# Optimization experiments

Hardware: AMD Instinct MI355X
Metric: run time of the kernel (lower is better)

## Reference

```python
import jax, jax.numpy as jnp
import numpy as np

N, E, G = 100000, 800000, 1000
N_IN, NHID, HEADS, NOUT = 128, 32, 4, 768
HC = NHID * HEADS


def setup_inputs() -> dict:
    key = jax.random.key(0)
    ks = jax.random.split(key, 12)
    s = 1.0 / np.sqrt(N_IN)
    inp = {
        "x": jax.random.normal(ks[0], (N, N_IN), jnp.float32),
        "edge_index": jax.random.randint(ks[1], (2, E), 0, N, jnp.int64),
        "batch": jnp.sort(jax.random.randint(ks[2], (N,), 0, G, jnp.int64)),
        "Wq": jax.random.uniform(ks[3], (N_IN, HC), jnp.float32, -s, s),
        "bq": jnp.zeros((HC,), jnp.float32),
        "Wk": jax.random.uniform(ks[4], (N_IN, HC), jnp.float32, -s, s),
        "bk": jnp.zeros((HC,), jnp.float32),
        "Wv": jax.random.uniform(ks[5], (N_IN, HC), jnp.float32, -s, s),
        "bv": jnp.zeros((HC,), jnp.float32),
        "Wskip": jax.random.uniform(ks[6], (N_IN, HC), jnp.float32, -s, s),
        "bskip": jnp.zeros((HC,), jnp.float32),
        "Wbeta": jax.random.uniform(ks[7], (3 * HC, 1), jnp.float32, -1.0 / np.sqrt(3 * HC), 1.0 / np.sqrt(3 * HC)),
        "W2": jax.random.uniform(ks[8], (HC, NOUT), jnp.float32, -1.0 / np.sqrt(HC), 1.0 / np.sqrt(HC)),
        "b2": jnp.zeros((NOUT,), jnp.float32),
    }
    return inp


def _transformer_net(x, edge_index, batch, Wq, bq, Wk, bk, Wv, bv, Wskip, bskip, Wbeta, W2, b2):
    src, dst = edge_index[0], edge_index[1]  # messages src -> dst
    q = (x @ Wq + bq).reshape(N, HEADS, NHID)
    k = (x @ Wk + bk).reshape(N, HEADS, NHID)
    v = (x @ Wv + bv).reshape(N, HEADS, NHID)
    # edge-wise attention logits [E, H]
    alpha = jnp.einsum('ehc,ehc->eh', q[dst], k[src]) / np.sqrt(NHID)
    # segment softmax over incoming edges of each destination node
    m = jax.ops.segment_max(alpha, dst, num_segments=N)  # [N, H]
    e = jnp.exp(alpha - m[dst])
    denom = jax.ops.segment_sum(e, dst, num_segments=N)  # [N, H]
    attn = e / (denom[dst] + 1e-16)  # [E, H]
    msg = v[src] * attn[..., None]  # [E, H, C]
    out = jax.ops.segment_sum(msg, dst, num_segments=N).reshape(N, HC)
    # beta gating (root skip)
    skip = x @ Wskip + bskip  # [N, HC]
    beta = jax.nn.sigmoid(jnp.concatenate([out, skip, out - skip], axis=-1) @ Wbeta)  # [N, 1]
    out = beta * skip + (1.0 - beta) * out
    # LeakyReLU (default slope 0.01)
    out = jnp.where(out >= 0, out, 0.01 * out)
    # global mean pool per graph
    sums = jax.ops.segment_sum(out, batch, num_segments=G)  # [G, HC]
    cnts = jax.ops.segment_sum(jnp.ones((N,), out.dtype), batch, num_segments=G)
    pooled = sums / jnp.maximum(cnts, 1.0)[:, None]
    return pooled @ W2 + b2  # [G, NOUT]


def reference(x, edge_index, batch, Wq, bq, Wk, bk, Wv, bv, Wskip, bskip, Wbeta, W2, b2):
    return _transformer_net(x, edge_index, batch, Wq, bq, Wk, bk, Wv, bv, Wskip, bskip, Wbeta, W2, b2)
```

## Files before the change

### kernel.cpp

```cpp
#include <hip/hip_runtime.h>
#include <hip/hip_bf16.h>
#include <math.h>

#define NIN 128
#define HC 128
#define NOUT 768

typedef __attribute__((ext_vector_type(8))) short bf16x8;
typedef __attribute__((ext_vector_type(4))) float f32x4;
typedef __attribute__((ext_vector_type(4))) unsigned short ushort4v;
typedef __attribute__((ext_vector_type(8))) unsigned short ushort8v;

__device__ __forceinline__ unsigned short f2bf(float f) {
    __hip_bfloat16 h = __float2bfloat16(f);
    return *(unsigned short*)&h;
}

__device__ __forceinline__ float bfe(ushort8v u, int j) {
    return __uint_as_float(((unsigned int)u[j]) << 16);
}

__global__ __launch_bounds__(256) void prep_w(
    const float* __restrict__ Wq, const float* __restrict__ Wk,
    const float* __restrict__ Wv, const float* __restrict__ Wsk,
    unsigned short* __restrict__ Wtb)
{
    const float* W = (blockIdx.x == 0) ? Wq : (blockIdx.x == 1) ? Wk
                   : (blockIdx.x == 2) ? Wv : Wsk;
    unsigned short* out = Wtb + (size_t)blockIdx.x * 128 * 128;
    const int t = threadIdx.x;
    for (int s = 0; s < 16; ++s) {
        const int f = t + s * 256;
        const int k = f >> 5;
        const int n = (f & 31) * 4;
        float4 w4 = *(const float4*)(W + (size_t)k * 128 + n);
        out[(size_t)(n    ) * 128 + k] = f2bf(w4.x);
        out[(size_t)(n + 1) * 128 + k] = f2bf(w4.y);
        out[(size_t)(n + 2) * 128 + k] = f2bf(w4.z);
        out[(size_t)(n + 3) * 128 + k] = f2bf(w4.w);
    }
}

__global__ __launch_bounds__(256, 4) void gemm_kv(
    const float* __restrict__ x, const unsigned short* __restrict__ Wtb,
    const float* __restrict__ bk, const float* __restrict__ bv,
    __hip_bfloat16* __restrict__ kv, int N)
{
    __shared__ unsigned short At[128][136];
    const int tid = threadIdx.x;
    const int lane = tid & 63;
    const int wave = tid >> 6;
    const int rowBase = blockIdx.x * 128;
    const bool full = (rowBase + 128 <= N);

    #pragma unroll
    for (int s = 0; s < 16; ++s) {
        const int f = tid + s * 256;
        const int r = f >> 5;
        const int cl = (f & 31) * 4;
        const int gr = rowBase + r;
        float4 a4 = make_float4(0.f, 0.f, 0.f, 0.f);
        if (full || gr < N) a4 = *(const float4*)(x + (size_t)gr * 128 + cl);
        ushort4v u;
        u.x = f2bf(a4.x); u.y = f2bf(a4.y); u.z = f2bf(a4.z); u.w = f2bf(a4.w);
        *(ushort4v*)&At[r][cl] = u;
    }
    __syncthreads();

    bf16x8 afr[2][4];
    #pragma unroll
    for (int m = 0; m < 2; ++m)
        #pragma unroll
        for (int kk = 0; kk < 4; ++kk)
            afr[m][kk] = *(bf16x8*)&At[wave * 32 + m * 16 + (lane & 15)]
                                    [kk * 32 + (lane >> 4) * 8];

    const int colb = lane & 15;
    const int kofs = (lane >> 4) * 8;
    const int g4   = (lane >> 4) * 4;

    #pragma unroll
    for (int w2 = 0; w2 < 2; ++w2) {
        const unsigned short* Wp = Wtb + (size_t)(1 + w2) * 128 * 128;
        const float* bias = (w2 == 0) ? bk : bv;
        const int halfOfs = w2 * 128;

        f32x4 acc[2][8];
        #pragma unroll
        for (int m = 0; m < 2; ++m)
            #pragma unroll
            for (int nr = 0; nr < 8; ++nr)
                acc[m][nr] = (f32x4){0.f, 0.f, 0.f, 0.f};

        #pragma unroll
        for (int nr = 0; nr < 8; ++nr) {
            bf16x8 bfr[4];
            #pragma unroll
            for (int kk = 0; kk < 4; ++kk)
                bfr[kk] = *(const bf16x8*)(Wp + (size_t)(nr * 16 + colb) * 128
                                               + kk * 32 + kofs);
            #pragma unroll
            for (int kk = 0; kk < 4; ++kk) {
                #pragma unroll
                for (int m = 0; m < 2; ++m)
                    acc[m][nr] = __builtin_amdgcn_mfma_f32_16x16x32_bf16(
                        bfr[kk], afr[m][kk], acc[m][nr], 0, 0, 0);
            }
        }

        #pragma unroll
        for (int m = 0; m < 2; ++m) {
            const int xrow = rowBase + wave * 32 + m * 16 + (lane & 15);
            if (full || xrow < N) {
                #pragma unroll
                for (int nr = 0; nr < 8; ++nr) {
                    const int colb4 = nr * 16 + g4;
                    const float4 b4 = *(const float4*)(bias + colb4);
                    ushort4v pk;
                    pk.x = f2bf(acc[m][nr][0] + b4.x);
                    pk.y = f2bf(acc[m][nr][1] + b4.y);
                    pk.z = f2bf(acc[m][nr][2] + b4.z);
                    pk.w = f2bf(acc[m][nr][3] + b4.w);
                    *(ushort4v*)(kv + (size_t)xrow * 256 + halfOfs + colb4) = pk;
                }
            }
        }
    }
}

__global__ __launch_bounds__(256) void hist_kernel(
    const int* __restrict__ ei, int* __restrict__ cnt, int E)
{
    const int e = blockIdx.x * 256 + threadIdx.x;
    if (e < E) atomicAdd(cnt + ei[E + e], 1);
}

__global__ __launch_bounds__(1024) void scan_part(
    const int* __restrict__ cnt, int* __restrict__ start,
    int* __restrict__ bsum, int N)
{
    __shared__ int wsum[16];
    const int tid = threadIdx.x;
    const int lane = tid & 63;
    const int w = tid >> 6;
    const int i = blockIdx.x * 1024 + tid;
    const int v = (i < N) ? cnt[i] : 0;
    int xv = v;
    #pragma unroll
    for (int off = 1; off < 64; off <<= 1) {
        const int y = __shfl_up(xv, off, 64);
        if (lane >= off) xv += y;
    }
    if (lane == 63) wsum[w] = xv;
    __syncthreads();
    if (tid < 16) {
        int y = wsum[tid];
        #pragma unroll
        for (int off = 1; off < 16; off <<= 1) {
            const int z = __shfl_up(y, off, 64);
            if (tid >= off) y += z;
        }
        wsum[tid] = y;
    }
    __syncthreads();
    const int excl = (w > 0 ? wsum[w - 1] : 0) + xv - v;
    if (i < N) start[i] = excl;
    if (tid == 1023) bsum[blockIdx.x] = wsum[15];
}

__global__ __launch_bounds__(256) void scan_add(
    int* __restrict__ start, int* __restrict__ cursor,
    const int* __restrict__ bsum, int N, int NB)
{
    __shared__ int pref;
    const int i = blockIdx.x * 256 + threadIdx.x;
    const int chunk = (blockIdx.x * 256) >> 10;
    if (threadIdx.x == 0) {
        int s = 0;
        for (int b = 0; b < chunk; ++b) s += bsum[b];
        pref = s;
    }
    __syncthreads();
    if (i < N) {
        const int s = start[i] + pref;
        start[i] = s;
        cursor[i] = s;
    }
}

__global__ __launch_bounds__(256) void scatter_kernel(
    const int* __restrict__ ei, int* __restrict__ cursor,
    int* __restrict__ csr_src, int E)
{
    const int e = blockIdx.x * 256 + threadIdx.x;
    if (e < E) {
        const int d = ei[E + e];
        const int pos = atomicAdd(cursor + d, 1);
        csr_src[pos] = ei[e];
    }
}

__global__ __launch_bounds__(256) void node_aggr_fused(
    const float* __restrict__ x, const unsigned short* __restrict__ Wtb,
    const float* __restrict__ bq, const float* __restrict__ bsk,
    const __hip_bfloat16* __restrict__ kv,
    const int* __restrict__ start, const int* __restrict__ cnt,
    const int* __restrict__ csr_src, const float* __restrict__ Wbeta,
    __hip_bfloat16* __restrict__ gout, int N)
{
    __shared__ unsigned short At[16][136];
    __shared__ float q_lds[16][132];
    __shared__ float sk_lds[16][132];

    const int tid = threadIdx.x;
    const int lane = tid & 63;
    const int wave = tid >> 6;
    const int n0 = blockIdx.x * 16;

    #pragma unroll
    for (int s = 0; s < 2; ++s) {
        const int f = tid + s * 256;
        const int r = f >> 5;
        const int cl = (f & 31) * 4;
        const int gr = n0 + r;
        float4 a4 = make_float4(0.f, 0.f, 0.f, 0.f);
        if (gr < N) a4 = *(const float4*)(x + (size_t)gr * 128 + cl);
        ushort4v u;
        u.x = f2bf(a4.x); u.y = f2bf(a4.y); u.z = f2bf(a4.z); u.w = f2bf(a4.w);
        *(ushort4v*)&At[r][cl] = u;
    }
    __syncthreads();

    {
        bf16x8 afr[4];
        #pragma unroll
        for (int kk = 0; kk < 4; ++kk)
            afr[kk] = *(bf16x8*)&At[lane & 15][kk * 32 + (lane >> 4) * 8];
        const int colb = lane & 15;
        const int kofs = (lane >> 4) * 8;
        const int g4m  = (lane >> 4) * 4;
        const int rm   = lane & 15;

        f32x4 acc[2][2];
        #pragma unroll
        for (int a = 0; a < 2; ++a)
            #pragma unroll
            for (int b = 0; b < 2; ++b)
                acc[a][b] = (f32x4){0.f, 0.f, 0.f, 0.f};

        #pragma unroll
        for (int nr2 = 0; nr2 < 2; ++nr2) {
            const int nr = wave * 2 + nr2;
            #pragma unroll
            for (int wsel = 0; wsel < 2; ++wsel) {
                const unsigned short* Wp = Wtb + (size_t)(wsel == 0 ? 0 : 3) * 128 * 128;
                bf16x8 bfr[4];
                #pragma unroll
                for (int kk = 0; kk < 4; ++kk)
                    bfr[kk] = *(const bf16x8*)(Wp + (size_t)(nr * 16 + colb) * 128
                                                   + kk * 32 + kofs);
                #pragma unroll
                for (int kk = 0; kk < 4; ++kk)
                    acc[wsel][nr2] = __builtin_amdgcn_mfma_f32_16x16x32_bf16(
                        bfr[kk], afr[kk], acc[wsel][nr2], 0, 0, 0);
            }
        }

        #pragma unroll
        for (int nr2 = 0; nr2 < 2; ++nr2) {
            const int col = (wave * 2 + nr2) * 16 + g4m;
            #pragma unroll
            for (int j = 0; j < 4; ++j) {
                q_lds[rm][col + j]  = acc[0][nr2][j] + bq[col + j];
                sk_lds[rm][col + j] = acc[1][nr2][j] + bsk[col + j];
            }
        }
    }
    __syncthreads();

    const int g  = lane >> 4;
    const int t  = lane & 15;
    const int ch = t * 8;
    const int r  = wave * 4 + g;
    const int n  = n0 + r;
    const bool nok = (n < N);
    const float scale = 0.17677669529663687f;

    float qv[8];
    {
        float4 q0 = *(float4*)&q_lds[r][ch];
        float4 q1 = *(float4*)&q_lds[r][ch + 4];
        qv[0]=q0.x; qv[1]=q0.y; qv[2]=q0.z; qv[3]=q0.w;
        qv[4]=q1.x; qv[5]=q1.y; qv[6]=q1.z; qv[7]=q1.w;
    }

    const int s0v = nok ? start[n] : 0;
    const int e1v = nok ? s0v + cnt[n] : 0;
    float den = 0.f;
    float acc[8];
    #pragma unroll
    for (int j = 0; j < 8; ++j) acc[j] = 0.f;

    for (int base = s0v; base < e1v; base += 16) {
        const int nblk = min(16, e1v - base);
        const int sidx = csr_src[base + min(t, nblk - 1)];
        int j = 0;
        for (; j + 1 < nblk; j += 2) {
            const int sa = __shfl(sidx, g * 16 + j,     64);
            const int sb = __shfl(sidx, g * 16 + j + 1, 64);
            const ushort8v k8a = *(const ushort8v*)(kv + (size_t)sa * 256 + ch);
            const ushort8v v8a = *(const ushort8v*)(kv + (size_t)sa * 256 + 128 + ch);
            const ushort8v k8b = *(const ushort8v*)(kv + (size_t)sb * 256 + ch);
            const ushort8v v8b = *(const ushort8v*)(kv + (size_t)sb * 256 + 128 + ch);
            float pa = 0.f, pb = 0.f;
            #pragma unroll
            for (int jj = 0; jj < 8; ++jj) {
                pa = fmaf(bfe(k8a, jj), qv[jj], pa);
                pb = fmaf(bfe(k8b, jj), qv[jj], pb);
            }
            pa += __shfl_xor(pa, 1, 64);
            pa += __shfl_xor(pa, 2, 64);
            pb += __shfl_xor(pb, 1, 64);
            pb += __shfl_xor(pb, 2, 64);
            const float exa = __expf(pa * scale);
            const float exb = __expf(pb * scale);
            den += exa + exb;
            #pragma unroll
            for (int jj = 0; jj < 8; ++jj)
                acc[jj] = fmaf(bfe(v8a, jj), exa, fmaf(bfe(v8b, jj), exb, acc[jj]));
        }
        if (j < nblk) {
            const int sa = __shfl(sidx, g * 16 + j, 64);
            const ushort8v k8a = *(const ushort8v*)(kv + (size_t)sa * 256 + ch);
            const ushort8v v8a = *(const ushort8v*)(kv + (size_t)sa * 256 + 128 + ch);
            float pa = 0.f;
            #pragma unroll
            for (int jj = 0; jj < 8; ++jj) pa = fmaf(bfe(k8a, jj), qv[jj], pa);
            pa += __shfl_xor(pa, 1, 64);
            pa += __shfl_xor(pa, 2, 64);
            const float exa = __expf(pa * scale);
            den += exa;
            #pragma unroll
            for (int jj = 0; jj < 8; ++jj) acc[jj] = fmaf(bfe(v8a, jj), exa, acc[jj]);
        }
    }

    const float inv = 1.f / (den + 1e-16f);
    float o[8], sk[8];
    {
        float4 s0f = *(float4*)&sk_lds[r][ch];
        float4 s1f = *(float4*)&sk_lds[r][ch + 4];
        sk[0]=s0f.x; sk[1]=s0f.y; sk[2]=s0f.z; sk[3]=s0f.w;
        sk[4]=s1f.x; sk[5]=s1f.y; sk[6]=s1f.z; sk[7]=s1f.w;
    }
    float part = 0.f;
    #pragma unroll
    for (int j = 0; j < 8; ++j) {
        o[j] = acc[j] * inv;
        part += o[j] * Wbeta[ch + j] + sk[j] * Wbeta[HC + ch + j]
              + (o[j] - sk[j]) * Wbeta[2 * HC + ch + j];
    }
    part += __shfl_xor(part, 1, 64);
    part += __shfl_xor(part, 2, 64);
    part += __shfl_xor(part, 4, 64);
    part += __shfl_xor(part, 8, 64);

    const float beta = 1.f / (1.f + __expf(-part));
    if (nok) {
        union { unsigned short h[8]; ushort8v v8; } pk;
        #pragma unroll
        for (int j = 0; j < 8; ++j) {
            float rv = beta * sk[j] + (1.f - beta) * o[j];
            rv = (rv >= 0.f) ? rv : 0.01f * rv;
            pk.h[j] = f2bf(rv);
        }
        *(ushort8v*)(gout + (size_t)n * HC + ch) = pk.v8;
    }
}

__global__ __launch_bounds__(256) void pool_final(
    const __hip_bfloat16* __restrict__ gout, const int* __restrict__ batch,
    const float* __restrict__ W2, const float* __restrict__ b2,
    float* __restrict__ out, int N, int G)
{
    const int g0 = blockIdx.x * 4;
    __shared__ float p[4][HC];
    const int wave = threadIdx.x >> 6;
    const int lane = threadIdx.x & 63;
    const int g = g0 + wave;
    if (g < G) {
        int lo = 0, hi = N;
        while (lo < hi) { const int m = (lo + hi) >> 1; if (batch[m] < g) lo = m + 1; else hi = m; }
        int lo2 = lo, hi2 = N;
        while (lo2 < hi2) { const int m = (lo2 + hi2) >> 1; if (batch[m] < g + 1) lo2 = m + 1; else hi2 = m; }
        float a0 = 0.f, a1 = 0.f;
        for (int r = lo; r < lo2; ++r) {
            const __hip_bfloat162 g2 = *(const __hip_bfloat162*)(gout + (size_t)r * HC + 2 * lane);
            a0 += __bfloat162float(g2.x);
            a1 += __bfloat162float(g2.y);
        }
        const float invc = 1.f / fmaxf((float)(lo2 - lo), 1.f);
        p[wave][2 * lane]     = a0 * invc;
        p[wave][2 * lane + 1] = a1 * invc;
    }
    __syncthreads();
    const int t = threadIdx.x;
    for (int j = t; j < NOUT; j += 256) {
        const float bj = b2[j];
        float a0 = bj, a1 = bj, a2 = bj, a3 = bj;
        #pragma unroll 4
        for (int c = 0; c < HC; ++c) {
            const float w = W2[(size_t)c * NOUT + j];
            a0 = fmaf(p[0][c], w, a0);
            a1 = fmaf(p[1][c], w, a1);
            a2 = fmaf(p[2][c], w, a2);
            a3 = fmaf(p[3][c], w, a3);
        }
        if (g0     < G) out[(size_t)(g0    ) * NOUT + j] = a0;
        if (g0 + 1 < G) out[(size_t)(g0 + 1) * NOUT + j] = a1;
        if (g0 + 2 < G) out[(size_t)(g0 + 2) * NOUT + j] = a2;
        if (g0 + 3 < G) out[(size_t)(g0 + 3) * NOUT + j] = a3;
    }
}

extern "C" void kernel_launch(void* const* d_in, const int* in_sizes, int n_in,
                              void* d_out, int out_size, void* d_ws, size_t ws_size,
                              hipStream_t stream) {
    const float* x     = (const float*)d_in[0];
    const int*   ei    = (const int*)d_in[1];
    const int*   batch = (const int*)d_in[2];
    const float* Wq  = (const float*)d_in[3];  const float* bq  = (const float*)d_in[4];
    const float* Wk  = (const float*)d_in[5];  const float* bk  = (const float*)d_in[6];
    const float* Wv  = (const float*)d_in[7];  const float* bv  = (const float*)d_in[8];
    const float* Wsk = (const float*)d_in[9];  const float* bsk = (const float*)d_in[10];
    const float* Wbeta = (const float*)d_in[11];
    const float* W2  = (const float*)d_in[12]; const float* b2  = (const float*)d_in[13];

    const int N = in_sizes[0] / NIN;
    const int E = in_sizes[1] / 2;
    const int G = out_size / NOUT;

    char* ws = (char*)d_ws;
    const size_t nbQ = (size_t)N * HC * sizeof(__hip_bfloat16);
    __hip_bfloat16* kv = (__hip_bfloat16*)(ws);
    char* p0 = ws + 2 * nbQ;
    unsigned short* Wtb = (unsigned short*)p0;            p0 += 4 * 128 * 128 * sizeof(unsigned short);
    int* cnt    = (int*)p0;                               p0 += (size_t)N * sizeof(int);
    int* start  = (int*)p0;                               p0 += (size_t)N * sizeof(int);
    int* cursor = (int*)p0;                               p0 += (size_t)N * sizeof(int);
    int* bsum   = (int*)p0;                               p0 += 1024 * sizeof(int);
    int* csr    = (int*)p0;                               p0 += (size_t)E * sizeof(int);
    __hip_bfloat16* gout = (__hip_bfloat16*)p0;

    hipMemsetAsync(cnt, 0, (size_t)N * sizeof(int), stream);

    const int eb = (E + 255) / 256;
    const int NB = (N + 1023) / 1024;
    hist_kernel<<<eb, 256, 0, stream>>>(ei, cnt, E);
    scan_part<<<NB, 1024, 0, stream>>>(cnt, start, bsum, N);
    scan_add<<<(N + 255) / 256, 256, 0, stream>>>(start, cursor, bsum, N, NB);
    scatter_kernel<<<eb, 256, 0, stream>>>(ei, cursor, csr, E);

    prep_w<<<4, 256, 0, stream>>>(Wq, Wk, Wv, Wsk, Wtb);
    gemm_kv<<<(N + 127) / 128, 256, 0, stream>>>(x, Wtb, bk, bv, kv, N);

    node_aggr_fused<<<(N + 15) / 16, 256, 0, stream>>>(x, Wtb, bq, bsk, kv,
                                                       start, cnt, csr, Wbeta,
                                                       gout, N);

    pool_final<<<(G + 3) / 4, 256, 0, stream>>>(gout, batch, W2, b2,
                                                (float*)d_out, N, G);
}
```

Baseline: 326.5 us.

## Merge weight prep with histogram and GEMM with CSR scatter; store q/skip as bf16 in LDS

Folds the weight transpose/cast into the edge histogram launch, and runs the CSR scatter as extra blocks of the K/V GEMM launch, cutting launches and letting independent work overlap. Also stores q and skip in LDS as bf16 rather than fp32, roughly halving LDS use in the aggregation kernel, which may raise occupancy. Rounding q and skip to bf16 adds precision loss. Scatter blocks also sit in a kernel whose launch bounds and LDS size were set for the GEMM.

```diff
diff --git a/kernel.cpp b/kernel.cpp
--- a/kernel.cpp
+++ b/kernel.cpp
@@ -19,34 +19,109 @@
 __device__ __forceinline__ float bfe(ushort8v u, int j) {
     return __uint_as_float(((unsigned int)u[j]) << 16);
 }
-
-__global__ __launch_bounds__(256) void prep_w(
+__device__ __forceinline__ float bfe4(ushort4v u, int j) {
+    return __uint_as_float(((unsigned int)u[j]) << 16);
+}
+
+__global__ __launch_bounds__(256) void prep_hist(
     const float* __restrict__ Wq, const float* __restrict__ Wk,
     const float* __restrict__ Wv, const float* __restrict__ Wsk,
-    unsigned short* __restrict__ Wtb)
-{
-    const float* W = (blockIdx.x == 0) ? Wq : (blockIdx.x == 1) ? Wk
-                   : (blockIdx.x == 2) ? Wv : Wsk;
-    unsigned short* out = Wtb + (size_t)blockIdx.x * 128 * 128;
-    const int t = threadIdx.x;
-    for (int s = 0; s < 16; ++s) {
-        const int f = t + s * 256;
-        const int k = f >> 5;
-        const int n = (f & 31) * 4;
-        float4 w4 = *(const float4*)(W + (size_t)k * 128 + n);
-        out[(size_t)(n    ) * 128 + k] = f2bf(w4.x);
-        out[(size_t)(n + 1) * 128 + k] = f2bf(w4.y);
-        out[(size_t)(n + 2) * 128 + k] = f2bf(w4.z);
-        out[(size_t)(n + 3) * 128 + k] = f2bf(w4.w);
-    }
-}
-
-__global__ __launch_bounds__(256, 4) void gemm_kv(
+    unsigned short* __restrict__ Wtb,
+    const int* __restrict__ ei, int* __restrict__ cnt, int E)
+{
+    if (blockIdx.x < 4) {
+        const float* W = (blockIdx.x == 0) ? Wq : (blockIdx.x == 1) ? Wk
+                       : (blockIdx.x == 2) ? Wv : Wsk;
+        unsigned short* out = Wtb + (size_t)blockIdx.x * 128 * 128;
+        const int t = threadIdx.x;
+        for (int s = 0; s < 16; ++s) {
+            const int f = t + s * 256;
+            const int k = f >> 5;
+            const int n = (f & 31) * 4;
+            float4 w4 = *(const float4*)(W + (size_t)k * 128 + n);
+            out[(size_t)(n    ) * 128 + k] = f2bf(w4.x);
+            out[(size_t)(n + 1) * 128 + k] = f2bf(w4.y);
+            out[(size_t)(n + 2) * 128 + k] = f2bf(w4.z);
+            out[(size_t)(n + 3) * 128 + k] = f2bf(w4.w);
+        }
+    } else {
+        const int e = (blockIdx.x - 4) * 256 + threadIdx.x;
+        if (e < E) atomicAdd(cnt + ei[E + e], 1);
+    }
+}
+
+__global__ __launch_bounds__(1024) void scan_part(
+    const int* __restrict__ cnt, int* __restrict__ start,
+    int* __restrict__ bsum, int N)
+{
+    __shared__ int wsum[16];
+    const int tid = threadIdx.x;
+    const int lane = tid & 63;
+    const int w = tid >> 6;
+    const int i = blockIdx.x * 1024 + tid;
+    const int v = (i < N) ? cnt[i] : 0;
+    int xv = v;
+    #pragma unroll
+    for (int off = 1; off < 64; off <<= 1) {
+        const int y = __shfl_up(xv, off, 64);
+        if (lane >= off) xv += y;
+    }
+    if (lane == 63) wsum[w] = xv;
+    __syncthreads();
+    if (tid < 16) {
+        int y = wsum[tid];
+        #pragma unroll
+        for (int off = 1; off < 16; off <<= 1) {
+            const int z = __shfl_up(y, off, 64);
+            if (tid >= off) y += z;
+        }
+        wsum[tid] = y;
+    }
+    __syncthreads();
+    const int excl = (w > 0 ? wsum[w - 1] : 0) + xv - v;
+    if (i < N) start[i] = excl;
+    if (tid == 1023) bsum[blockIdx.x] = wsum[15];
+}
+
+__global__ __launch_bounds__(256) void scan_add(
+    int* __restrict__ start, int* __restrict__ cursor,
+    const int* __restrict__ bsum, int N, int NB)
+{
+    __shared__ int pref;
+    const int i = blockIdx.x * 256 + threadIdx.x;
+    const int chunk = (blockIdx.x * 256) >> 10;
+    if (threadIdx.x == 0) {
+        int s = 0;
+        for (int b = 0; b < chunk; ++b) s += bsum[b];
+        pref = s;
+    }
+    __syncthreads();
+    if (i < N) {
+        const int s = start[i] + pref;
+        start[i] = s;
+        cursor[i] = s;
+    }
+}
+
+__global__ __launch_bounds__(256, 4) void gemm_scatter(
     const float* __restrict__ x, const unsigned short* __restrict__ Wtb,
     const float* __restrict__ bk, const float* __restrict__ bv,
-    __hip_bfloat16* __restrict__ kv, int N)
+    __hip_bfloat16* __restrict__ kv, int N,
+    const int* __restrict__ ei, int* __restrict__ cursor,
+    int* __restrict__ csr_src, int E, int nGemm)
 {
     __shared__ unsigned short At[128][136];
+
+    if ((int)blockIdx.x >= nGemm) {
+        const int e = (blockIdx.x - nGemm) * 256 + threadIdx.x;
+        if (e < E) {
+            const int d = ei[E + e];
+            const int pos = atomicAdd(cursor + d, 1);
+            csr_src[pos] = ei[e];
+        }
+        return;
+    }
+
     const int tid = threadIdx.x;
     const int lane = tid & 63;
     const int wave = tid >> 6;
@@ -128,78 +203,6 @@
     }
 }
 
-__global__ __launch_bounds__(256) void hist_kernel(
-    const int* __restrict__ ei, int* __restrict__ cnt, int E)
-{
-    const int e = blockIdx.x * 256 + threadIdx.x;
-    if (e < E) atomicAdd(cnt + ei[E + e], 1);
-}
-
-__global__ __launch_bounds__(1024) void scan_part(
-    const int* __restrict__ cnt, int* __restrict__ start,
-    int* __restrict__ bsum, int N)
-{
-    __shared__ int wsum[16];
-    const int tid = threadIdx.x;
-    const int lane = tid & 63;
-    const int w = tid >> 6;
-    const int i = blockIdx.x * 1024 + tid;
-    const int v = (i < N) ? cnt[i] : 0;
-    int xv = v;
-    #pragma unroll
-    for (int off = 1; off < 64; off <<= 1) {
-        const int y = __shfl_up(xv, off, 64);
-        if (lane >= off) xv += y;
-    }
-    if (lane == 63) wsum[w] = xv;
-    __syncthreads();
-    if (tid < 16) {
-        int y = wsum[tid];
-        #pragma unroll
-        for (int off = 1; off < 16; off <<= 1) {
-            const int z = __shfl_up(y, off, 64);
-            if (tid >= off) y += z;
-        }
-        wsum[tid] = y;
-    }
-    __syncthreads();
-    const int excl = (w > 0 ? wsum[w - 1] : 0) + xv - v;
-    if (i < N) start[i] = excl;
-    if (tid == 1023) bsum[blockIdx.x] = wsum[15];
-}
-
-__global__ __launch_bounds__(256) void scan_add(
-    int* __restrict__ start, int* __restrict__ cursor,
-    const int* __restrict__ bsum, int N, int NB)
-{
-    __shared__ int pref;
-    const int i = blockIdx.x * 256 + threadIdx.x;
-    const int chunk = (blockIdx.x * 256) >> 10;
-    if (threadIdx.x == 0) {
-        int s = 0;
-        for (int b = 0; b < chunk; ++b) s += bsum[b];
-        pref = s;
-    }
-    __syncthreads();
-    if (i < N) {
-        const int s = start[i] + pref;
-        start[i] = s;
-        cursor[i] = s;
-    }
-}
-
-__global__ __launch_bounds__(256) void scatter_kernel(
-    const int* __restrict__ ei, int* __restrict__ cursor,
-    int* __restrict__ csr_src, int E)
-{
-    const int e = blockIdx.x * 256 + threadIdx.x;
-    if (e < E) {
-        const int d = ei[E + e];
-        const int pos = atomicAdd(cursor + d, 1);
-        csr_src[pos] = ei[e];
-    }
-}
-
 __global__ __launch_bounds__(256) void node_aggr_fused(
     const float* __restrict__ x, const unsigned short* __restrict__ Wtb,
     const float* __restrict__ bq, const float* __restrict__ bsk,
@@ -209,8 +212,8 @@
     __hip_bfloat16* __restrict__ gout, int N)
 {
     __shared__ unsigned short At[16][136];
-    __shared__ float q_lds[16][132];
-    __shared__ float sk_lds[16][132];
+    __shared__ unsigned short q_l[16][136];
+    __shared__ unsigned short sk_l[16][136];
 
     const int tid = threadIdx.x;
     const int lane = tid & 63;
@@ -269,11 +272,14 @@
         #pragma unroll
         for (int nr2 = 0; nr2 < 2; ++nr2) {
             const int col = (wave * 2 + nr2) * 16 + g4m;
+            ushort4v qp, sp;
             #pragma unroll
             for (int j = 0; j < 4; ++j) {
-                q_lds[rm][col + j]  = acc[0][nr2][j] + bq[col + j];
-                sk_lds[rm][col + j] = acc[1][nr2][j] + bsk[col + j];
+                qp[j] = f2bf(acc[0][nr2][j] + bq[col + j]);
+                sp[j] = f2bf(acc[1][nr2][j] + bsk[col + j]);
             }
+            *(ushort4v*)&q_l[rm][col]  = qp;
+            *(ushort4v*)&sk_l[rm][col] = sp;
         }
     }
     __syncthreads();
@@ -288,10 +294,9 @@
 
     float qv[8];
     {
-        float4 q0 = *(float4*)&q_lds[r][ch];
-        float4 q1 = *(float4*)&q_lds[r][ch + 4];
-        qv[0]=q0.x; qv[1]=q0.y; qv[2]=q0.z; qv[3]=q0.w;
-        qv[4]=q1.x; qv[5]=q1.y; qv[6]=q1.z; qv[7]=q1.w;
+        const ushort8v q8 = *(const ushort8v*)&q_l[r][ch];
+        #pragma unroll
+        for (int j = 0; j < 8; ++j) qv[j] = bfe(q8, j);
     }
 
     const int s0v = nok ? start[n] : 0;
@@ -348,10 +353,9 @@
     const float inv = 1.f / (den + 1e-16f);
     float o[8], sk[8];
     {
-        float4 s0f = *(float4*)&sk_lds[r][ch];
-        float4 s1f = *(float4*)&sk_lds[r][ch + 4];
-        sk[0]=s0f.x; sk[1]=s0f.y; sk[2]=s0f.z; sk[3]=s0f.w;
-        sk[4]=s1f.x; sk[5]=s1f.y; sk[6]=s1f.z; sk[7]=s1f.w;
+        const ushort8v s8 = *(const ushort8v*)&sk_l[r][ch];
+        #pragma unroll
+        for (int j = 0; j < 8; ++j) sk[j] = bfe(s8, j);
     }
     float part = 0.f;
     #pragma unroll
@@ -456,13 +460,13 @@
 
     const int eb = (E + 255) / 256;
     const int NB = (N + 1023) / 1024;
-    hist_kernel<<<eb, 256, 0, stream>>>(ei, cnt, E);
+    const int nGemm = (N + 127) / 128;
+
+    prep_hist<<<4 + eb, 256, 0, stream>>>(Wq, Wk, Wv, Wsk, Wtb, ei, cnt, E);
     scan_part<<<NB, 1024, 0, stream>>>(cnt, start, bsum, N);
     scan_add<<<(N + 255) / 256, 256, 0, stream>>>(start, cursor, bsum, N, NB);
-    scatter_kernel<<<eb, 256, 0, stream>>>(ei, cursor, csr, E);
-
-    prep_w<<<4, 256, 0, stream>>>(Wq, Wk, Wv, Wsk, Wtb);
-    gemm_kv<<<(N + 127) / 128, 256, 0, stream>>>(x, Wtb, bk, bv, kv, N);
+    gemm_scatter<<<nGemm + eb, 256, 0, stream>>>(x, Wtb, bk, bv, kv, N,
+                                                 ei, cursor, csr, E, nGemm);
 
     node_aggr_fused<<<(N + 15) / 16, 256, 0, stream>>>(x, Wtb, bq, bsk, kv,
                                                        start, cnt, csr, Wbeta,
```

Result: faster. 266.1 us (-18.5%).
